# Performance work log

Hardware: AMD Instinct MI355X
Metric: run time of the kernel (lower is better)

## Reference

```python
import jax, jax.numpy as jnp
import numpy as np

BATCH, DIM, HID, T = 1024, 1024, 4096, 16


def setup_inputs() -> dict:
    key = jax.random.key(0)
    k1, k2, k3 = jax.random.split(key, 3)
    # small init scale keeps the tanh-MLP dynamics stable over t in [0, 1]
    return {
        "y_init": jax.random.normal(k1, (BATCH, DIM), dtype=jnp.float32),
        "t_span": jnp.linspace(0.0, 1.0, T, dtype=jnp.float32),
        "W1": jax.random.normal(k2, (DIM, HID), dtype=jnp.float32) * 0.02,
        "b1": jnp.zeros((HID,), dtype=jnp.float32),
        "W2": jax.random.normal(k3, (HID, DIM), dtype=jnp.float32) * 0.02,
        "b2": jnp.zeros((DIM,), dtype=jnp.float32),
    }


def _vf(t, y, W1, b1, W2, b2):
    # vector field f(t, y): 2-layer tanh MLP, [B, D] -> [B, D]
    return jnp.tanh(y @ W1 + b1) @ W2 + b2


def _solve(y_init, t_span, W1, b1, W2, b2):
    # Fixed-grid RK4 solve over consecutive t_span points -> traj [T, B, D]
    def rk4(y, ts):
        t0, t1 = ts
        h = t1 - t0
        k1 = _vf(t0, y, W1, b1, W2, b2)
        k2 = _vf(t0 + h * 0.5, y + h * 0.5 * k1, W1, b1, W2, b2)
        k3 = _vf(t0 + h * 0.5, y + h * 0.5 * k2, W1, b1, W2, b2)
        k4 = _vf(t1, y + h * k3, W1, b1, W2, b2)
        y_next = y + (h / 6.0) * (k1 + 2.0 * k2 + 2.0 * k3 + k4)
        return y_next, y_next

    _, ys = jax.lax.scan(rk4, y_init, (t_span[:-1], t_span[1:]))
    return jnp.concatenate([y_init[None], ys], axis=0)


def reference(y_init, t_span, W1, b1, W2, b2):
    traj = _solve(y_init, t_span, W1, b1, W2, b2)
    return (t_span, traj)
```

## Files before the change

kernel.cpp:

```cpp
#include <hip/hip_runtime.h>
#include <hip/hip_bf16.h>
#include <stdint.h>

#define BATCH 1024
#define DIM   1024
#define HID   4096
#define TPTS  16

typedef __attribute__((ext_vector_type(8))) short  short8;
typedef __attribute__((ext_vector_type(4))) float  floatx4;

__device__ __forceinline__ unsigned short f32_to_bf16_bits(float f) {
    union { float f; unsigned u; } v; v.f = f;
    return (unsigned short)((v.u + 0x7fffu + ((v.u >> 16) & 1u)) >> 16);
}

__device__ __forceinline__ void store_bf16x4(unsigned short* p, floatx4 v) {
    union { unsigned short u[4]; uint2 q; } pk;
    pk.u[0] = f32_to_bf16_bits(v[0]);
    pk.u[1] = f32_to_bf16_bits(v[1]);
    pk.u[2] = f32_to_bf16_bits(v[2]);
    pk.u[3] = f32_to_bf16_bits(v[3]);
    *(uint2*)p = pk.q;
}

__device__ __forceinline__ float fast_tanh(float x) {
    float e = __expf(2.0f * x);
    return 1.0f - 2.0f / (e + 1.0f);
}

__device__ __forceinline__ void g2l16(const unsigned short* g, char* l) {
    __builtin_amdgcn_global_load_lds(
        (const __attribute__((address_space(1))) void*)g,
        (__attribute__((address_space(3))) void*)l, 16, 0, 0);
}

template<int MODE>
__global__ __launch_bounds__(256, 2)
void gemm_bt(const unsigned short* __restrict__ A,
             const unsigned short* __restrict__ Bt,
             const float* __restrict__ bias,
             void* __restrict__ Cout,
             int lda, int ldb, int ldc, int K, long long partStride)
{
    __shared__ __align__(16) char smem[49152];

    const int tid  = threadIdx.x;
    const int wave = tid >> 6;
    const int lane = tid & 63;
    const int wn = wave * 32;
    const int lr = lane & 15;
    const int q  = lane >> 4;

    int rowBase, colBase, zIdx;
    if (MODE == 1) {
        const int lin = (int)blockIdx.x + ((int)blockIdx.y << 5);
        const int swz = ((lin & 7) << 6) | (lin >> 3);
        colBase = (swz >> 4) << 7;
        rowBase = (swz & 15) << 6;
        zIdx = 0;
    } else {
        const int lin = (int)blockIdx.x +
                        (((int)blockIdx.y + ((int)blockIdx.z << 4)) << 3);
        const int swz = ((lin & 7) << 6) | (lin >> 3);
        zIdx = swz >> 7;
        const int s = swz & 127;
        colBase = (s & 7) << 7;
        rowBase = (s >> 3) << 6;
    }
    const long long koff = (long long)zIdx * K;

    const unsigned short* gp[6];
    int lo[6];
#pragma unroll
    for (int j = 0; j < 6; ++j) {
        const int p  = (j * 256 + tid) * 16;
        const int pa = (j < 2) ? p : (p - 8192);
        const int row = pa >> 7;
        const int ch  = (pa >> 4) & 7;
        const int sc  = ch ^ (row & 7);
        if (j < 2)
            gp[j] = A + (long long)(rowBase + row) * lda + koff + sc * 8;
        else
            gp[j] = Bt + (long long)(colBase + row) * ldb + koff + sc * 8;
        lo[j] = p;
    }

    floatx4 acc[4][2];
#pragma unroll
    for (int mi = 0; mi < 4; ++mi)
#pragma unroll
        for (int ni = 0; ni < 2; ++ni) {
            floatx4 z4 = {0.f, 0.f, 0.f, 0.f};
            acc[mi][ni] = z4;
        }

    const int xr = lr & 7;
    int aOff[4], bOff[2];
#pragma unroll
    for (int i = 0; i < 4; ++i) aOff[i] = (i * 16 + lr) * 128;
#pragma unroll
    for (int i = 0; i < 2; ++i) bOff[i] = (wn + i * 16 + lr) * 128;
    const int swz0 = ((0 + q) ^ xr) * 16;
    const int swz1 = ((4 + q) ^ xr) * 16;

    const int KB = K >> 6;

#pragma unroll
    for (int j = 0; j < 6; ++j)
        g2l16(gp[j], smem + lo[j]);
    __syncthreads();

    int cur = 0;
    for (int kb = 0; kb < KB; ++kb) {
        if (kb + 1 < KB) {
            const int kadv = (kb + 1) * 64;
            char* nb = smem + (cur ^ 1) * 24576;
#pragma unroll
            for (int j = 0; j < 6; ++j)
                g2l16(gp[j] + kadv, nb + lo[j]);
        }
        const char* sAb = smem + cur * 24576;
        const char* sBb = sAb + 8192;

        short8 af[4][2], bfr[2][2];
#pragma unroll
        for (int i = 0; i < 4; ++i) {
            af[i][0] = *(const short8*)(sAb + aOff[i] + swz0);
            af[i][1] = *(const short8*)(sAb + aOff[i] + swz1);
        }
#pragma unroll
        for (int i = 0; i < 2; ++i) {
            bfr[i][0] = *(const short8*)(sBb + bOff[i] + swz0);
            bfr[i][1] = *(const short8*)(sBb + bOff[i] + swz1);
        }
#pragma unroll
        for (int g = 0; g < 2; ++g)
#pragma unroll
            for (int mi = 0; mi < 4; ++mi)
#pragma unroll
                for (int ni = 0; ni < 2; ++ni)
                    acc[mi][ni] = __builtin_amdgcn_mfma_f32_16x16x32_bf16(
                        af[mi][g], bfr[ni][g], acc[mi][ni], 0, 0, 0);

        __syncthreads();
        cur ^= 1;
    }

    if (MODE == 1) {
        float bias2[2];
#pragma unroll
        for (int ni = 0; ni < 2; ++ni)
            bias2[ni] = bias[colBase + wn + ni * 16 + lr];
        unsigned short* sC = (unsigned short*)smem;
#pragma unroll
        for (int mi = 0; mi < 4; ++mi)
#pragma unroll
            for (int ni = 0; ni < 2; ++ni)
#pragma unroll
                for (int r = 0; r < 4; ++r) {
                    const int row = mi * 16 + q * 4 + r;
                    const int col = wn + ni * 16 + lr;
                    sC[row * 136 + col] =
                        f32_to_bf16_bits(fast_tanh(acc[mi][ni][r] + bias2[ni]));
                }
        __syncthreads();
        unsigned short* C = (unsigned short*)Cout;
#pragma unroll
        for (int it = 0; it < 4; ++it) {
            const int row = it * 16 + (tid >> 4);
            const int cc  = (tid & 15) * 8;
            *(uint4*)(C + (long long)(rowBase + row) * ldc + colBase + cc) =
                *(const uint4*)(sC + row * 136 + cc);
        }
    } else {
        float* C = (float*)Cout + (long long)zIdx * partStride;
#pragma unroll
        for (int mi = 0; mi < 4; ++mi)
#pragma unroll
            for (int ni = 0; ni < 2; ++ni) {
                const int r0 = rowBase + mi * 16 + q * 4;
                const int c  = colBase + wn + ni * 16 + lr;
#pragma unroll
                for (int r = 0; r < 4; ++r)
                    C[(long long)(r0 + r) * ldc + c] = acc[mi][ni][r];
            }
    }
}

__global__ void combine(const float* __restrict__ parts,
                        const float* __restrict__ b2,
                        const float* __restrict__ ycur,
                        const float* __restrict__ tspan,
                        int step, int mode,
                        float* __restrict__ kacc,
                        unsigned short* __restrict__ ybf,
                        float* __restrict__ ynext)
{
    const int i = blockIdx.x * blockDim.x + threadIdx.x;
    const float h = tspan[step + 1] - tspan[step];
    const int NV = BATCH * DIM / 4;
    const floatx4* p = (const floatx4*)parts;
    floatx4 k = p[i] + p[i + NV] + p[i + 2 * NV] + p[i + 3 * NV];
    k = k + *(const floatx4*)(b2 + ((i * 4) & (DIM - 1)));
    floatx4 y = ((const floatx4*)ycur)[i];
    floatx4* ka = (floatx4*)kacc;
    if (mode == 1) {
        ka[i] = k;
        store_bf16x4(ybf + i * 4, y + (0.5f * h) * k);
    } else if (mode == 2) {
        ka[i] = ka[i] + 2.0f * k;
        store_bf16x4(ybf + i * 4, y + (0.5f * h) * k);
    } else if (mode == 3) {
        ka[i] = ka[i] + 2.0f * k;
        store_bf16x4(ybf + i * 4, y + h * k);
    } else {
        floatx4 yn = y + (h * (1.0f / 6.0f)) * (ka[i] + k);
        ((floatx4*)ynext)[i] = yn;
        store_bf16x4(ybf + i * 4, yn);
    }
}

__global__ void transpose_cast(const float* __restrict__ in,
                               unsigned short* __restrict__ out, int R, int C)
{
    __shared__ float tile[32][33];
    const int bx = blockIdx.x * 32;
    const int by = blockIdx.y * 32;
    const int tx = threadIdx.x, ty = threadIdx.y;
#pragma unroll
    for (int i = 0; i < 4; ++i)
        tile[ty + i * 8][tx] = in[(long long)(by + ty + i * 8) * C + bx + tx];
    __syncthreads();
#pragma unroll
    for (int i = 0; i < 4; ++i)
        out[(long long)(bx + ty + i * 8) * R + by + tx] =
            f32_to_bf16_bits(tile[tx][ty + i * 8]);
}

__global__ void init_kernel(const float* __restrict__ y0,
                            const float* __restrict__ tspan,
                            float* __restrict__ out,
                            unsigned short* __restrict__ ybf)
{
    const int i = blockIdx.x * blockDim.x + threadIdx.x;
    floatx4 v = ((const floatx4*)y0)[i];
    ((floatx4*)(out + TPTS))[i] = v;
    store_bf16x4(ybf + i * 4, v);
    if (blockIdx.x == 0 && threadIdx.x < TPTS) out[threadIdx.x] = tspan[threadIdx.x];
}

extern "C" void kernel_launch(void* const* d_in, const int* in_sizes, int n_in,
                              void* d_out, int out_size, void* d_ws, size_t ws_size,
                              hipStream_t stream)
{
    (void)in_sizes; (void)n_in; (void)out_size; (void)ws_size;
    const float* y0    = (const float*)d_in[0];
    const float* tspan = (const float*)d_in[1];
    const float* W1    = (const float*)d_in[2];
    const float* b1    = (const float*)d_in[3];
    const float* W2    = (const float*)d_in[4];
    const float* b2    = (const float*)d_in[5];
    float* out = (float*)d_out;

    char* ws = (char*)d_ws;
    unsigned short* W1T = (unsigned short*)(ws);
    unsigned short* W2T = (unsigned short*)(ws + (8ll << 20));
    unsigned short* Ybf = (unsigned short*)(ws + (16ll << 20));
    unsigned short* Hbf = (unsigned short*)(ws + (18ll << 20));
    float* parts = (float*)(ws + (26ll << 20));
    float* kacc  = (float*)(ws + (42ll << 20));

    dim3 tb(32, 8);
    transpose_cast<<<dim3(HID / 32, DIM / 32), tb, 0, stream>>>(W1, W1T, DIM, HID);
    transpose_cast<<<dim3(DIM / 32, HID / 32), tb, 0, stream>>>(W2, W2T, HID, DIM);
    init_kernel<<<BATCH * DIM / 1024, 256, 0, stream>>>(y0, tspan, out, Ybf);

    float* traj = out + TPTS;
    for (int t = 0; t < TPTS - 1; ++t) {
        const float* ycur = traj + (long long)t * BATCH * DIM;
        float* ynext = traj + (long long)(t + 1) * BATCH * DIM;
        for (int e = 0; e < 4; ++e) {
            gemm_bt<1><<<dim3(HID / 128, BATCH / 64, 1), 256, 0, stream>>>(
                Ybf, W1T, b1, (void*)Hbf, DIM, DIM, HID, DIM, 0LL);
            gemm_bt<0><<<dim3(DIM / 128, BATCH / 64, 4), 256, 0, stream>>>(
                Hbf, W2T, nullptr, (void*)parts, HID, HID, DIM, HID / 4,
                (long long)BATCH * DIM);
            combine<<<BATCH * DIM / 1024, 256, 0, stream>>>(
                parts, b2, ycur, tspan, t, e + 1, kacc, Ybf, ynext);
        }
    }
}
```

Measured before the change: 2.276 ms.

## Fuse split-K reduction and RK4 combine into second GEMM via atomic tile counters

Removes the separate combine kernel. Each split-K GEMM block fences its partial output and increments a per-tile atomic counter, and the last of the four blocks for a tile sums the partials and applies the RK4 stage update for that tile. This saves 60 kernel launches and lets combine work overlap with other GEMM tiles. In exchange it adds fence and atomic overhead, and the partials are still written to global memory and read back.

```diff
diff --git a/kernel.cpp b/kernel.cpp
--- a/kernel.cpp
+++ b/kernel.cpp
@@ -41,7 +41,11 @@
              const unsigned short* __restrict__ Bt,
              const float* __restrict__ bias,
              void* __restrict__ Cout,
-             int lda, int ldb, int ldc, int K, long long partStride)
+             int lda, int ldb, int ldc, int K, long long partStride,
+             const float* __restrict__ b2, const float* __restrict__ ycur,
+             const float* __restrict__ tspan, int step, int mode,
+             float* __restrict__ kacc, unsigned short* __restrict__ ybf,
+             float* __restrict__ ynext, unsigned int* __restrict__ cnt)
 {
     __shared__ __align__(16) char smem[49152];
 
@@ -52,7 +56,7 @@
     const int lr = lane & 15;
     const int q  = lane >> 4;
 
-    int rowBase, colBase, zIdx;
+    int rowBase, colBase, zIdx, tileS = 0;
     if (MODE == 1) {
         const int lin = (int)blockIdx.x + ((int)blockIdx.y << 5);
         const int swz = ((lin & 7) << 6) | (lin >> 3);
@@ -64,9 +68,9 @@
                         (((int)blockIdx.y + ((int)blockIdx.z << 4)) << 3);
         const int swz = ((lin & 7) << 6) | (lin >> 3);
         zIdx = swz >> 7;
-        const int s = swz & 127;
-        colBase = (s & 7) << 7;
-        rowBase = (s >> 3) << 6;
+        tileS = swz & 127;
+        colBase = (tileS & 7) << 7;
+        rowBase = (tileS >> 3) << 6;
     }
     const long long koff = (long long)zIdx * K;
 
@@ -185,39 +189,44 @@
                 for (int r = 0; r < 4; ++r)
                     C[(long long)(r0 + r) * ldc + c] = acc[mi][ni][r];
             }
-    }
-}
-
-__global__ void combine(const float* __restrict__ parts,
-                        const float* __restrict__ b2,
-                        const float* __restrict__ ycur,
-                        const float* __restrict__ tspan,
-                        int step, int mode,
-                        float* __restrict__ kacc,
-                        unsigned short* __restrict__ ybf,
-                        float* __restrict__ ynext)
-{
-    const int i = blockIdx.x * blockDim.x + threadIdx.x;
-    const float h = tspan[step + 1] - tspan[step];
-    const int NV = BATCH * DIM / 4;
-    const floatx4* p = (const floatx4*)parts;
-    floatx4 k = p[i] + p[i + NV] + p[i + 2 * NV] + p[i + 3 * NV];
-    k = k + *(const floatx4*)(b2 + ((i * 4) & (DIM - 1)));
-    floatx4 y = ((const floatx4*)ycur)[i];
-    floatx4* ka = (floatx4*)kacc;
-    if (mode == 1) {
-        ka[i] = k;
-        store_bf16x4(ybf + i * 4, y + (0.5f * h) * k);
-    } else if (mode == 2) {
-        ka[i] = ka[i] + 2.0f * k;
-        store_bf16x4(ybf + i * 4, y + (0.5f * h) * k);
-    } else if (mode == 3) {
-        ka[i] = ka[i] + 2.0f * k;
-        store_bf16x4(ybf + i * 4, y + h * k);
-    } else {
-        floatx4 yn = y + (h * (1.0f / 6.0f)) * (ka[i] + k);
-        ((floatx4*)ynext)[i] = yn;
-        store_bf16x4(ybf + i * 4, yn);
+
+        __threadfence();
+        __syncthreads();
+        __shared__ unsigned int sOld;
+        if (tid == 0) sOld = atomicAdd(&cnt[tileS], 1u);
+        __syncthreads();
+        if ((sOld & 3u) == 3u) {
+            __threadfence();
+            const float h = tspan[step + 1] - tspan[step];
+            const floatx4* p = (const floatx4*)Cout;
+            const floatx4* yc = (const floatx4*)ycur;
+            floatx4* ka = (floatx4*)kacc;
+            floatx4* yn = (floatx4*)ynext;
+            const int NV4 = BATCH * DIM / 4;
+            const int cb4 = colBase >> 2;
+#pragma unroll
+            for (int it = 0; it < 8; ++it) {
+                const int v = it * 256 + tid;
+                const int i = (rowBase + (v >> 5)) * (DIM / 4) + cb4 + (v & 31);
+                floatx4 k = p[i] + p[i + NV4] + p[i + 2 * NV4] + p[i + 3 * NV4];
+                k = k + *(const floatx4*)(b2 + ((i * 4) & (DIM - 1)));
+                floatx4 y = yc[i];
+                if (mode == 1) {
+                    ka[i] = k;
+                    store_bf16x4(ybf + i * 4, y + (0.5f * h) * k);
+                } else if (mode == 2) {
+                    ka[i] = ka[i] + 2.0f * k;
+                    store_bf16x4(ybf + i * 4, y + (0.5f * h) * k);
+                } else if (mode == 3) {
+                    ka[i] = ka[i] + 2.0f * k;
+                    store_bf16x4(ybf + i * 4, y + h * k);
+                } else {
+                    floatx4 ynv = y + (h * (1.0f / 6.0f)) * (ka[i] + k);
+                    yn[i] = ynv;
+                    store_bf16x4(ybf + i * 4, ynv);
+                }
+            }
+        }
     }
 }
 
@@ -241,13 +250,15 @@
 __global__ void init_kernel(const float* __restrict__ y0,
                             const float* __restrict__ tspan,
                             float* __restrict__ out,
-                            unsigned short* __restrict__ ybf)
+                            unsigned short* __restrict__ ybf,
+                            unsigned int* __restrict__ cnt)
 {
     const int i = blockIdx.x * blockDim.x + threadIdx.x;
     floatx4 v = ((const floatx4*)y0)[i];
     ((floatx4*)(out + TPTS))[i] = v;
     store_bf16x4(ybf + i * 4, v);
     if (blockIdx.x == 0 && threadIdx.x < TPTS) out[threadIdx.x] = tspan[threadIdx.x];
+    if (blockIdx.x == 1 && threadIdx.x < 128) cnt[threadIdx.x] = 0u;
 }
 
 extern "C" void kernel_launch(void* const* d_in, const int* in_sizes, int n_in,
@@ -270,11 +281,12 @@
     unsigned short* Hbf = (unsigned short*)(ws + (18ll << 20));
     float* parts = (float*)(ws + (26ll << 20));
     float* kacc  = (float*)(ws + (42ll << 20));
+    unsigned int* cnt = (unsigned int*)(ws + (46ll << 20));
 
     dim3 tb(32, 8);
     transpose_cast<<<dim3(HID / 32, DIM / 32), tb, 0, stream>>>(W1, W1T, DIM, HID);
     transpose_cast<<<dim3(DIM / 32, HID / 32), tb, 0, stream>>>(W2, W2T, HID, DIM);
-    init_kernel<<<BATCH * DIM / 1024, 256, 0, stream>>>(y0, tspan, out, Ybf);
+    init_kernel<<<BATCH * DIM / 1024, 256, 0, stream>>>(y0, tspan, out, Ybf, cnt);
 
     float* traj = out + TPTS;
     for (int t = 0; t < TPTS - 1; ++t) {
@@ -282,12 +294,12 @@
         float* ynext = traj + (long long)(t + 1) * BATCH * DIM;
         for (int e = 0; e < 4; ++e) {
             gemm_bt<1><<<dim3(HID / 128, BATCH / 64, 1), 256, 0, stream>>>(
-                Ybf, W1T, b1, (void*)Hbf, DIM, DIM, HID, DIM, 0LL);
+                Ybf, W1T, b1, (void*)Hbf, DIM, DIM, HID, DIM, 0LL,
+                nullptr, nullptr, nullptr, 0, 0, nullptr, nullptr, nullptr, nullptr);
             gemm_bt<0><<<dim3(DIM / 128, BATCH / 64, 4), 256, 0, stream>>>(
                 Hbf, W2T, nullptr, (void*)parts, HID, HID, DIM, HID / 4,
-                (long long)BATCH * DIM);
-            combine<<<BATCH * DIM / 1024, 256, 0, stream>>>(
-                parts, b2, ycur, tspan, t, e + 1, kacc, Ybf, ynext);
-        }
-    }
-}
+                (long long)BATCH * DIM,
+                b2, ycur, tspan, t, e + 1, kacc, Ybf, ynext, cnt);
+        }
+    }
+}
```

New measurement: 7.291 ms. +220.3%, slower.

## Fuse RK4 combine step into first GEMM via grid-wide barrier

Applied to the files above, without the earlier changes.

The separate combine kernel is folded into the prologue of the first GEMM. Each of the 512 blocks does its slice of the stage combination, writes the bf16 state with system-scope stores, and waits on a global atomic counter barrier before loading A with system-scope loads. This removes one kernel launch per stage. In exchange it relies on all 512 blocks being co-resident, and the A tile is now loaded through registers with uncached atomic loads instead of direct global-to-LDS copies.

```diff
diff --git a/kernel.cpp b/kernel.cpp
--- a/kernel.cpp
+++ b/kernel.cpp
@@ -6,9 +6,11 @@
 #define DIM   1024
 #define HID   4096
 #define TPTS  16
+#define NBLK  512
 
 typedef __attribute__((ext_vector_type(8))) short  short8;
 typedef __attribute__((ext_vector_type(4))) float  floatx4;
+typedef __attribute__((ext_vector_type(2))) unsigned long long u64x2;
 
 __device__ __forceinline__ unsigned short f32_to_bf16_bits(float f) {
     union { float f; unsigned u; } v; v.f = f;
@@ -24,6 +26,25 @@
     *(uint2*)p = pk.q;
 }
 
+__device__ __forceinline__ void st_sys_bf16x4(unsigned short* p, floatx4 v) {
+    union { unsigned short u[4]; unsigned long long q; } pk;
+    pk.u[0] = f32_to_bf16_bits(v[0]);
+    pk.u[1] = f32_to_bf16_bits(v[1]);
+    pk.u[2] = f32_to_bf16_bits(v[2]);
+    pk.u[3] = f32_to_bf16_bits(v[3]);
+    __hip_atomic_store((unsigned long long*)p, pk.q,
+                       __ATOMIC_RELAXED, __HIP_MEMORY_SCOPE_SYSTEM);
+}
+
+__device__ __forceinline__ u64x2 ld_sys16b(const unsigned short* p) {
+    u64x2 r;
+    r.x = __hip_atomic_load((const unsigned long long*)p,
+                            __ATOMIC_RELAXED, __HIP_MEMORY_SCOPE_SYSTEM);
+    r.y = __hip_atomic_load((const unsigned long long*)p + 1,
+                            __ATOMIC_RELAXED, __HIP_MEMORY_SCOPE_SYSTEM);
+    return r;
+}
+
 __device__ __forceinline__ float fast_tanh(float x) {
     float e = __expf(2.0f * x);
     return 1.0f - 2.0f / (e + 1.0f);
@@ -35,16 +56,178 @@
         (__attribute__((address_space(3))) void*)l, 16, 0, 0);
 }
 
-template<int MODE>
 __global__ __launch_bounds__(256, 2)
-void gemm_bt(const unsigned short* __restrict__ A,
-             const unsigned short* __restrict__ Bt,
-             const float* __restrict__ bias,
-             void* __restrict__ Cout,
-             int lda, int ldb, int ldc, int K, long long partStride)
+void g1_fused(const unsigned short* __restrict__ W1T,
+              const float* __restrict__ b1,
+              const float* __restrict__ b2,
+              const float* __restrict__ tspan,
+              unsigned short* __restrict__ Ybf,
+              unsigned short* __restrict__ Hbf,
+              const float* __restrict__ parts,
+              float* __restrict__ kacc,
+              float* __restrict__ traj,
+              unsigned* __restrict__ bar,
+              unsigned tgt, int cstep, int cmode)
 {
     __shared__ __align__(16) char smem[49152];
-
+    const int tid  = threadIdx.x;
+    const int bid  = (int)blockIdx.x;
+
+    if (cmode) {
+        const float h = tspan[cstep + 1] - tspan[cstep];
+        const floatx4* pp = (const floatx4*)parts;
+        const floatx4* yc = (const floatx4*)(traj + (long long)cstep * BATCH * DIM);
+        floatx4* yn = (floatx4*)(traj + (long long)(cstep + 1) * BATCH * DIM);
+        floatx4* ka = (floatx4*)kacc;
+        const int NV4 = BATCH * DIM / 4;
+#pragma unroll
+        for (int u = 0; u < 2; ++u) {
+            const int i = (bid << 9) + tid * 2 + u;
+            floatx4 k = pp[i] + pp[i + NV4] + pp[i + 2 * NV4] + pp[i + 3 * NV4];
+            k = k + *(const floatx4*)(b2 + ((i * 4) & (DIM - 1)));
+            floatx4 y = yc[i];
+            floatx4 ynew;
+            if (cmode == 1)      { ka[i] = k;               ynew = y + (0.5f * h) * k; }
+            else if (cmode == 2) { ka[i] = ka[i] + 2.0f * k; ynew = y + (0.5f * h) * k; }
+            else if (cmode == 3) { ka[i] = ka[i] + 2.0f * k; ynew = y + h * k; }
+            else { ynew = y + (h * (1.0f / 6.0f)) * (ka[i] + k); yn[i] = ynew; }
+            st_sys_bf16x4(Ybf + i * 4, ynew);
+        }
+        __syncthreads();
+        if (tid == 0) {
+            __hip_atomic_fetch_add(bar, 1u, __ATOMIC_RELAXED,
+                                   __HIP_MEMORY_SCOPE_AGENT);
+            while (__hip_atomic_load(bar, __ATOMIC_RELAXED,
+                                     __HIP_MEMORY_SCOPE_AGENT) < tgt)
+                __builtin_amdgcn_s_sleep(2);
+        }
+        __syncthreads();
+        asm volatile("" ::: "memory");
+    }
+
+    const int wave = tid >> 6;
+    const int lane = tid & 63;
+    const int wn = wave * 32;
+    const int lr = lane & 15;
+    const int q  = lane >> 4;
+
+    const int swz = ((bid & 7) << 6) | (bid >> 3);
+    const int colBase = (swz >> 4) << 7;
+    const int rowBase = (swz & 15) << 6;
+
+    const unsigned short* gpA[2]; const unsigned short* gpB[4];
+    int loA[2], loB[4];
+#pragma unroll
+    for (int j = 0; j < 6; ++j) {
+        const int p  = (j * 256 + tid) * 16;
+        const int pa = (j < 2) ? p : (p - 8192);
+        const int row = pa >> 7;
+        const int ch  = (pa >> 4) & 7;
+        const int sc  = ch ^ (row & 7);
+        if (j < 2) { gpA[j] = Ybf + (long long)(rowBase + row) * DIM + sc * 8; loA[j] = p; }
+        else { gpB[j - 2] = W1T + (long long)(colBase + row) * DIM + sc * 8; loB[j - 2] = p; }
+    }
+
+    floatx4 acc[4][2];
+#pragma unroll
+    for (int mi = 0; mi < 4; ++mi)
+#pragma unroll
+        for (int ni = 0; ni < 2; ++ni) {
+            floatx4 z4 = {0.f, 0.f, 0.f, 0.f};
+            acc[mi][ni] = z4;
+        }
+
+    const int xr = lr & 7;
+    int aOff[4], bOff[2];
+#pragma unroll
+    for (int i = 0; i < 4; ++i) aOff[i] = (i * 16 + lr) * 128;
+#pragma unroll
+    for (int i = 0; i < 2; ++i) bOff[i] = (wn + i * 16 + lr) * 128;
+    const int swz0 = ((0 + q) ^ xr) * 16;
+    const int swz1 = ((4 + q) ^ xr) * 16;
+
+    u64x2 a0 = ld_sys16b(gpA[0]);
+    u64x2 a1 = ld_sys16b(gpA[1]);
+#pragma unroll
+    for (int j = 0; j < 4; ++j) g2l16(gpB[j], smem + loB[j]);
+    *(u64x2*)(smem + loA[0]) = a0;
+    *(u64x2*)(smem + loA[1]) = a1;
+    __syncthreads();
+
+    int cur = 0;
+    for (int kb = 0; kb < 16; ++kb) {
+        u64x2 na0, na1;
+        char* nb = smem + (cur ^ 1) * 24576;
+        if (kb + 1 < 16) {
+            const int kadv = (kb + 1) * 64;
+            na0 = ld_sys16b(gpA[0] + kadv);
+            na1 = ld_sys16b(gpA[1] + kadv);
+#pragma unroll
+            for (int j = 0; j < 4; ++j) g2l16(gpB[j] + kadv, nb + loB[j]);
+        }
+        const char* sAb = smem + cur * 24576;
+        const char* sBb = sAb + 8192;
+
+        short8 af[4][2], bfr[2][2];
+#pragma unroll
+        for (int i = 0; i < 4; ++i) {
+            af[i][0] = *(const short8*)(sAb + aOff[i] + swz0);
+            af[i][1] = *(const short8*)(sAb + aOff[i] + swz1);
+        }
+#pragma unroll
+        for (int i = 0; i < 2; ++i) {
+            bfr[i][0] = *(const short8*)(sBb + bOff[i] + swz0);
+            bfr[i][1] = *(const short8*)(sBb + bOff[i] + swz1);
+        }
+#pragma unroll
+        for (int g = 0; g < 2; ++g)
+#pragma unroll
+            for (int mi = 0; mi < 4; ++mi)
+#pragma unroll
+                for (int ni = 0; ni < 2; ++ni)
+                    acc[mi][ni] = __builtin_amdgcn_mfma_f32_16x16x32_bf16(
+                        af[mi][g], bfr[ni][g], acc[mi][ni], 0, 0, 0);
+
+        if (kb + 1 < 16) {
+            *(u64x2*)(nb + loA[0]) = na0;
+            *(u64x2*)(nb + loA[1]) = na1;
+        }
+        __syncthreads();
+        cur ^= 1;
+    }
+
+    float bias2[2];
+#pragma unroll
+    for (int ni = 0; ni < 2; ++ni)
+        bias2[ni] = b1[colBase + wn + ni * 16 + lr];
+    unsigned short* sC = (unsigned short*)smem;
+#pragma unroll
+    for (int mi = 0; mi < 4; ++mi)
+#pragma unroll
+        for (int ni = 0; ni < 2; ++ni)
+#pragma unroll
+            for (int r = 0; r < 4; ++r) {
+                const int row = mi * 16 + q * 4 + r;
+                const int col = wn + ni * 16 + lr;
+                sC[row * 136 + col] =
+                    f32_to_bf16_bits(fast_tanh(acc[mi][ni][r] + bias2[ni]));
+            }
+    __syncthreads();
+#pragma unroll
+    for (int it = 0; it < 4; ++it) {
+        const int row = it * 16 + (tid >> 4);
+        const int cc  = (tid & 15) * 8;
+        *(uint4*)(Hbf + (long long)(rowBase + row) * HID + colBase + cc) =
+            *(const uint4*)(sC + row * 136 + cc);
+    }
+}
+
+__global__ __launch_bounds__(256, 2)
+void gemm2_bt(const unsigned short* __restrict__ A,
+              const unsigned short* __restrict__ Bt,
+              float* __restrict__ Cout)
+{
+    __shared__ __align__(16) char smem[49152];
     const int tid  = threadIdx.x;
     const int wave = tid >> 6;
     const int lane = tid & 63;
@@ -52,23 +235,14 @@
     const int lr = lane & 15;
     const int q  = lane >> 4;
 
-    int rowBase, colBase, zIdx;
-    if (MODE == 1) {
-        const int lin = (int)blockIdx.x + ((int)blockIdx.y << 5);
-        const int swz = ((lin & 7) << 6) | (lin >> 3);
-        colBase = (swz >> 4) << 7;
-        rowBase = (swz & 15) << 6;
-        zIdx = 0;
-    } else {
-        const int lin = (int)blockIdx.x +
-                        (((int)blockIdx.y + ((int)blockIdx.z << 4)) << 3);
-        const int swz = ((lin & 7) << 6) | (lin >> 3);
-        zIdx = swz >> 7;
-        const int s = swz & 127;
-        colBase = (s & 7) << 7;
-        rowBase = (s >> 3) << 6;
-    }
-    const long long koff = (long long)zIdx * K;
+    const int lin = (int)blockIdx.x +
+                    (((int)blockIdx.y + ((int)blockIdx.z << 4)) << 3);
+    const int swz = ((lin & 7) << 6) | (lin >> 3);
+    const int zIdx  = swz >> 7;
+    const int tileS = swz & 127;
+    const int colBase = (tileS & 7) << 7;
+    const int rowBase = (tileS >> 3) << 6;
+    const long long koff = (long long)zIdx * 1024;
 
     const unsigned short* gp[6];
     int lo[6];
@@ -80,9 +254,9 @@
         const int ch  = (pa >> 4) & 7;
         const int sc  = ch ^ (row & 7);
         if (j < 2)
-            gp[j] = A + (long long)(rowBase + row) * lda + koff + sc * 8;
+            gp[j] = A + (long long)(rowBase + row) * HID + koff + sc * 8;
         else
-            gp[j] = Bt + (long long)(colBase + row) * ldb + koff + sc * 8;
+            gp[j] = Bt + (long long)(colBase + row) * HID + koff + sc * 8;
         lo[j] = p;
     }
 
@@ -104,16 +278,14 @@
     const int swz0 = ((0 + q) ^ xr) * 16;
     const int swz1 = ((4 + q) ^ xr) * 16;
 
-    const int KB = K >> 6;
-
 #pragma unroll
     for (int j = 0; j < 6; ++j)
         g2l16(gp[j], smem + lo[j]);
     __syncthreads();
 
     int cur = 0;
-    for (int kb = 0; kb < KB; ++kb) {
-        if (kb + 1 < KB) {
+    for (int kb = 0; kb < 16; ++kb) {
+        if (kb + 1 < 16) {
             const int kadv = (kb + 1) * 64;
             char* nb = smem + (cur ^ 1) * 24576;
 #pragma unroll
@@ -147,45 +319,17 @@
         cur ^= 1;
     }
 
-    if (MODE == 1) {
-        float bias2[2];
-#pragma unroll
-        for (int ni = 0; ni < 2; ++ni)
-            bias2[ni] = bias[colBase + wn + ni * 16 + lr];
-        unsigned short* sC = (unsigned short*)smem;
-#pragma unroll
-        for (int mi = 0; mi < 4; ++mi)
-#pragma unroll
-            for (int ni = 0; ni < 2; ++ni)
-#pragma unroll
-                for (int r = 0; r < 4; ++r) {
-                    const int row = mi * 16 + q * 4 + r;
-                    const int col = wn + ni * 16 + lr;
-                    sC[row * 136 + col] =
-                        f32_to_bf16_bits(fast_tanh(acc[mi][ni][r] + bias2[ni]));
-                }
-        __syncthreads();
-        unsigned short* C = (unsigned short*)Cout;
-#pragma unroll
-        for (int it = 0; it < 4; ++it) {
-            const int row = it * 16 + (tid >> 4);
-            const int cc  = (tid & 15) * 8;
-            *(uint4*)(C + (long long)(rowBase + row) * ldc + colBase + cc) =
-                *(const uint4*)(sC + row * 136 + cc);
-        }
-    } else {
-        float* C = (float*)Cout + (long long)zIdx * partStride;
-#pragma unroll
-        for (int mi = 0; mi < 4; ++mi)
-#pragma unroll
-            for (int ni = 0; ni < 2; ++ni) {
-                const int r0 = rowBase + mi * 16 + q * 4;
-                const int c  = colBase + wn + ni * 16 + lr;
-#pragma unroll
-                for (int r = 0; r < 4; ++r)
-                    C[(long long)(r0 + r) * ldc + c] = acc[mi][ni][r];
-            }
-    }
+    float* C = Cout + (long long)zIdx * (BATCH * DIM);
+#pragma unroll
+    for (int mi = 0; mi < 4; ++mi)
+#pragma unroll
+        for (int ni = 0; ni < 2; ++ni) {
+            const int r0 = rowBase + mi * 16 + q * 4;
+            const int c  = colBase + wn + ni * 16 + lr;
+#pragma unroll
+            for (int r = 0; r < 4; ++r)
+                C[(long long)(r0 + r) * DIM + c] = acc[mi][ni][r];
+        }
 }
 
 __global__ void combine(const float* __restrict__ parts,
@@ -205,16 +349,7 @@
     k = k + *(const floatx4*)(b2 + ((i * 4) & (DIM - 1)));
     floatx4 y = ((const floatx4*)ycur)[i];
     floatx4* ka = (floatx4*)kacc;
-    if (mode == 1) {
-        ka[i] = k;
-        store_bf16x4(ybf + i * 4, y + (0.5f * h) * k);
-    } else if (mode == 2) {
-        ka[i] = ka[i] + 2.0f * k;
-        store_bf16x4(ybf + i * 4, y + (0.5f * h) * k);
-    } else if (mode == 3) {
-        ka[i] = ka[i] + 2.0f * k;
-        store_bf16x4(ybf + i * 4, y + h * k);
-    } else {
+    if (mode == 4) {
         floatx4 yn = y + (h * (1.0f / 6.0f)) * (ka[i] + k);
         ((floatx4*)ynext)[i] = yn;
         store_bf16x4(ybf + i * 4, yn);
@@ -241,13 +376,15 @@
 __global__ void init_kernel(const float* __restrict__ y0,
                             const float* __restrict__ tspan,
                             float* __restrict__ out,
-                            unsigned short* __restrict__ ybf)
+                            unsigned short* __restrict__ ybf,
+                            unsigned int* __restrict__ bar)
 {
     const int i = blockIdx.x * blockDim.x + threadIdx.x;
     floatx4 v = ((const floatx4*)y0)[i];
     ((floatx4*)(out + TPTS))[i] = v;
     store_bf16x4(ybf + i * 4, v);
     if (blockIdx.x == 0 && threadIdx.x < TPTS) out[threadIdx.x] = tspan[threadIdx.x];
+    if (blockIdx.x == 1 && threadIdx.x == 0) *bar = 0u;
 }
 
 extern "C" void kernel_launch(void* const* d_in, const int* in_sizes, int n_in,
@@ -270,24 +407,27 @@
     unsigned short* Hbf = (unsigned short*)(ws + (18ll << 20));
     float* parts = (float*)(ws + (26ll << 20));
     float* kacc  = (float*)(ws + (42ll << 20));
+    unsigned int* bar = (unsigned int*)(ws + (46ll << 20));
 
     dim3 tb(32, 8);
     transpose_cast<<<dim3(HID / 32, DIM / 32), tb, 0, stream>>>(W1, W1T, DIM, HID);
     transpose_cast<<<dim3(DIM / 32, HID / 32), tb, 0, stream>>>(W2, W2T, HID, DIM);
-    init_kernel<<<BATCH * DIM / 1024, 256, 0, stream>>>(y0, tspan, out, Ybf);
+    init_kernel<<<BATCH * DIM / 1024, 256, 0, stream>>>(y0, tspan, out, Ybf, bar);
 
     float* traj = out + TPTS;
+    unsigned k = 0;
     for (int t = 0; t < TPTS - 1; ++t) {
-        const float* ycur = traj + (long long)t * BATCH * DIM;
-        float* ynext = traj + (long long)(t + 1) * BATCH * DIM;
         for (int e = 0; e < 4; ++e) {
-            gemm_bt<1><<<dim3(HID / 128, BATCH / 64, 1), 256, 0, stream>>>(
-                Ybf, W1T, b1, (void*)Hbf, DIM, DIM, HID, DIM, 0LL);
-            gemm_bt<0><<<dim3(DIM / 128, BATCH / 64, 4), 256, 0, stream>>>(
-                Hbf, W2T, nullptr, (void*)parts, HID, HID, DIM, HID / 4,
-                (long long)BATCH * DIM);
-            combine<<<BATCH * DIM / 1024, 256, 0, stream>>>(
-                parts, b2, ycur, tspan, t, e + 1, kacc, Ybf, ynext);
-        }
-    }
-}
+            const int cmode = (k == 0) ? 0 : (int)(((k - 1) & 3u) + 1u);
+            const int cstep = (k == 0) ? 0 : (int)((k - 1) >> 2);
+            g1_fused<<<NBLK, 256, 0, stream>>>(W1T, b1, b2, tspan, Ybf, Hbf,
+                                               parts, kacc, traj, bar,
+                                               k * NBLK, cstep, cmode);
+            gemm2_bt<<<dim3(8, 16, 4), 256, 0, stream>>>(Hbf, W2T, parts);
+            ++k;
+        }
+    }
+    combine<<<BATCH * DIM / 1024, 256, 0, stream>>>(
+        parts, b2, traj + 14LL * BATCH * DIM, tspan, 14, 4, kacc, Ybf,
+        traj + 15LL * BATCH * DIM);
+}
```

New measurement: 3.563 ms. 56.5% more time.
